# Kernel tuning notes

Hardware: AMD Instinct MI355X
Metric: run time of the kernel (lower is better)

## Reference

```python
import jax, jax.numpy as jnp
import numpy as np

INPUT_CHANNELS = 64
OUT_CHANNELS = 64
OUT_DIM = 4
IN_FEAT = INPUT_CHANNELS * OUT_DIM * 2   # 512
OUT_FEAT = OUT_CHANNELS * OUT_DIM        # 256
BATCH = 65536


def setup_inputs() -> dict:
    key = jax.random.key(0)
    k_x, k_w, k_b = jax.random.split(key, 3)
    x = jax.random.normal(k_x, (BATCH, IN_FEAT), dtype=jnp.float32)
    weight = jax.random.normal(k_w, (OUT_FEAT, IN_FEAT), dtype=jnp.float32)
    bias = jax.random.normal(k_b, (1, OUT_FEAT), dtype=jnp.float32)
    return {"x": x, "weight": weight, "bias": bias}


def reference(x, weight, bias) -> jnp.ndarray:
    # Original: (x[:, None] * weight).sum(-1) / sqrt(input_channels) + 0.1*bias
    # Mathematically identical to a GEMM: x @ weight.T
    scale = 1.0 / jnp.sqrt(jnp.asarray(INPUT_CHANNELS, dtype=x.dtype))
    out = jnp.einsum('bi,oi->bo', x, weight) * scale  # [B, out_feat]
    out = out + bias * 0.1
    return out
```

## Files before the change

kernel.cpp:

```cpp
#include <hip/hip_runtime.h>
#include <hip/hip_bf16.h>


typedef __bf16 bf16;
typedef __attribute__((ext_vector_type(8))) __bf16 bf16x8;
typedef __attribute__((ext_vector_type(4))) __bf16 bf16x4;
typedef __attribute__((ext_vector_type(4))) float f32x4;

#define BATCH_ 65536
#define KDIM   512
#define NDIM   256
#define NHALF  128
#define CHUNK_ROWS 16
#define CHUNKS 8
#define ROWS_PER_BLOCK (CHUNK_ROWS * CHUNKS)
#define OPAD 132

__global__ __launch_bounds__(256) void wcvt_kernel(const float* __restrict__ w,
                                                   bf16* __restrict__ wb) {
    int i = (blockIdx.x * 256 + threadIdx.x) * 4;
    f32x4 v = *(const f32x4*)(w + i);
    bf16x4 o;
    o[0] = (bf16)(v.x * 0.125f);
    o[1] = (bf16)(v.y * 0.125f);
    o[2] = (bf16)(v.z * 0.125f);
    o[3] = (bf16)(v.w * 0.125f);
    *(bf16x4*)(wb + i) = o;
}

__device__ __forceinline__ void stage_issue(const float* xc, int tid, f32x4 (&r)[4]) {
#pragma unroll
    for (int i = 0; i < 4; ++i)
        r[i] = *(const f32x4*)((const char*)xc + i * 8192 + tid * 16);
}

__device__ __forceinline__ void stage_write(bf16* buf, int tid, const f32x4 (&r)[4]) {
#pragma unroll
    for (int i = 0; i < 4; ++i) {
        const int row = i * 4 + (tid >> 7);
        const int off = (tid & 127) * 8;
        const int phys = row * 1024 + (off ^ ((row & 7) << 4));
        bf16x4 o;
        o[0] = (bf16)r[i].x;
        o[1] = (bf16)r[i].y;
        o[2] = (bf16)r[i].z;
        o[3] = (bf16)r[i].w;
        *(bf16x4*)((char*)buf + phys) = o;
    }
}

__device__ __forceinline__ void compute_chunk(const bf16* buf, const bf16x8 (&wf)[16],
                                              int l16, int q, f32x4& acc) {
    acc = (f32x4)0.0f;
    const char* base = (const char*)buf + l16 * 1024;
    const int xo = (l16 & 7) << 4;
#pragma unroll
    for (int kc = 0; kc < 16; ++kc) {
        bf16x8 a = *(const bf16x8*)(base + ((kc * 64 + q * 16) ^ xo));
        acc = __builtin_amdgcn_mfma_f32_16x16x32_bf16(a, wf[kc], acc, 0, 0, 0);
    }
}

__device__ __forceinline__ void owrite(float* ob, int w, int l16, int q,
                                       const f32x4& acc) {
    float* p = ob + (q * 4) * OPAD + w * 16 + l16;
#pragma unroll
    for (int rr = 0; rr < 4; ++rr)
        p[rr * OPAD] = acc[rr];
}

__device__ __forceinline__ void ostore(const float* ob, float* __restrict__ out,
                                       long row0, int half, int tid,
                                       const f32x4& bvv) {
    const int r2 = tid >> 5;
    const int c4 = (tid & 31) * 4;
    f32x4 v = *(const f32x4*)(ob + r2 * OPAD + c4);
    v.x += bvv.x; v.y += bvv.y; v.z += bvv.z; v.w += bvv.w;
    *(f32x4*)(out + (row0 + r2) * NDIM + half * NHALF + c4) = v;
}

__device__ __forceinline__ void lds_barrier() {
    asm volatile("s_waitcnt lgkmcnt(0)" ::: "memory");
    __builtin_amdgcn_s_barrier();
    __builtin_amdgcn_sched_barrier(0);
}

__global__ __launch_bounds__(512, 4) void gemm_kernel(const float* __restrict__ x,
                                                      const bf16* __restrict__ wb,
                                                      const float* __restrict__ bias,
                                                      float* __restrict__ out) {
    __shared__ __align__(16) bf16 bufA[CHUNK_ROWS * KDIM];
    __shared__ __align__(16) bf16 bufB[CHUNK_ROWS * KDIM];
    __shared__ __align__(16) float obuf0[CHUNK_ROWS * OPAD];
    __shared__ __align__(16) float obuf1[CHUNK_ROWS * OPAD];

    const int tid  = threadIdx.x;
    const int lane = tid & 63;
    const int w    = tid >> 6;
    const int q    = lane >> 4;
    const int l16  = lane & 15;

    const int g    = blockIdx.x;
    const int half = (g >> 3) & 1;
    const long rb  = (long)((g & 7) | ((g >> 4) << 3));
    const int n0   = half * NHALF + w * 16;
    const long row_base = rb * ROWS_PER_BLOCK;

    bf16x8 wf[16];
#pragma unroll
    for (int kc = 0; kc < 16; ++kc)
        wf[kc] = *(const bf16x8*)(wb + (long)(n0 + l16) * KDIM + kc * 32 + q * 8);

    f32x4 bvv;
    {
        f32x4 b = *(const f32x4*)(bias + half * NHALF + (tid & 31) * 4);
        bvv.x = 0.1f * b.x; bvv.y = 0.1f * b.y;
        bvv.z = 0.1f * b.z; bvv.w = 0.1f * b.w;
    }

    const float* xblk = x + row_base * KDIM;

    f32x4 r[4];
    stage_issue(xblk, tid, r);
    stage_write(bufA, tid, r);
    lds_barrier();

    f32x4 acc;
#pragma unroll 1
    for (int t = 0; t < CHUNKS; t += 2) {
        if (t + 1 < CHUNKS)
            stage_issue(xblk + (long)(t + 1) * CHUNK_ROWS * KDIM, tid, r);
        compute_chunk(bufA, wf, l16, q, acc);
        owrite(obuf0, w, l16, q, acc);
        if (t + 1 < CHUNKS)
            stage_write(bufB, tid, r);
        lds_barrier();
        ostore(obuf0, out, row_base + (long)t * CHUNK_ROWS, half, tid, bvv);

        if (t + 2 < CHUNKS)
            stage_issue(xblk + (long)(t + 2) * CHUNK_ROWS * KDIM, tid, r);
        compute_chunk(bufB, wf, l16, q, acc);
        owrite(obuf1, w, l16, q, acc);
        if (t + 2 < CHUNKS)
            stage_write(bufA, tid, r);
        lds_barrier();
        ostore(obuf1, out, row_base + (long)(t + 1) * CHUNK_ROWS, half, tid, bvv);
    }
}

extern "C" void kernel_launch(void* const* d_in, const int* in_sizes, int n_in,
                              void* d_out, int out_size, void* d_ws, size_t ws_size,
                              hipStream_t stream) {
    const float* x    = (const float*)d_in[0];
    const float* w    = (const float*)d_in[1];
    const float* bias = (const float*)d_in[2];
    float* out = (float*)d_out;
    bf16* wb   = (bf16*)d_ws;

    wcvt_kernel<<<(NDIM * KDIM) / (256 * 4), 256, 0, stream>>>(w, wb);
    gemm_kernel<<<(BATCH_ / ROWS_PER_BLOCK) * 2, 512, 0, stream>>>(x, wb, bias, out);
}
```

Before: 223.4 us.

## Halve block threads; each wave computes two 16-col N tiles

Blocks shrink from 512 to 256 threads, and each wave now covers 32 output columns with two MFMA accumulators. Each A fragment read from LDS is reused for two MFMAs, which halves LDS reads per MFMA. Staging switches to 32-byte loads per thread with bf16x8 LDS writes, and the output store loops over two rows. The cost is twice the weight registers per thread (wf[16][2]), and fewer waves per block may cut latency hiding, which launch_bounds(256,2) tries to offset.

New measurement: 225.0 us. No clear change (+0.7%).

```diff
diff --git a/kernel.cpp b/kernel.cpp
--- a/kernel.cpp
+++ b/kernel.cpp
@@ -28,55 +28,65 @@
     *(bf16x4*)(wb + i) = o;
 }
 
-__device__ __forceinline__ void stage_issue(const float* xc, int tid, f32x4 (&r)[4]) {
+__device__ __forceinline__ void stage_issue(const float* xc, int tid, f32x4 (&r)[8]) {
 #pragma unroll
-    for (int i = 0; i < 4; ++i)
-        r[i] = *(const f32x4*)((const char*)xc + i * 8192 + tid * 16);
-}
-
-__device__ __forceinline__ void stage_write(bf16* buf, int tid, const f32x4 (&r)[4]) {
-#pragma unroll
-    for (int i = 0; i < 4; ++i) {
-        const int row = i * 4 + (tid >> 7);
-        const int off = (tid & 127) * 8;
-        const int phys = row * 1024 + (off ^ ((row & 7) << 4));
-        bf16x4 o;
-        o[0] = (bf16)r[i].x;
-        o[1] = (bf16)r[i].y;
-        o[2] = (bf16)r[i].z;
-        o[3] = (bf16)r[i].w;
-        *(bf16x4*)((char*)buf + phys) = o;
+    for (int j = 0; j < 4; ++j) {
+        r[2 * j]     = *(const f32x4*)((const char*)xc + j * 8192 + tid * 32);
+        r[2 * j + 1] = *(const f32x4*)((const char*)xc + j * 8192 + tid * 32 + 16);
     }
 }
 
-__device__ __forceinline__ void compute_chunk(const bf16* buf, const bf16x8 (&wf)[16],
-                                              int l16, int q, f32x4& acc) {
-    acc = (f32x4)0.0f;
+__device__ __forceinline__ void stage_write(bf16* buf, int tid, const f32x4 (&r)[8]) {
+#pragma unroll
+    for (int j = 0; j < 4; ++j) {
+        const int row = j * 4 + (tid >> 6);
+        const int off = (tid & 63) * 16;
+        const int phys = row * 1024 + (off ^ ((row & 7) << 4));
+        bf16x8 o;
+        o[0] = (bf16)r[2 * j].x;     o[1] = (bf16)r[2 * j].y;
+        o[2] = (bf16)r[2 * j].z;     o[3] = (bf16)r[2 * j].w;
+        o[4] = (bf16)r[2 * j + 1].x; o[5] = (bf16)r[2 * j + 1].y;
+        o[6] = (bf16)r[2 * j + 1].z; o[7] = (bf16)r[2 * j + 1].w;
+        *(bf16x8*)((char*)buf + phys) = o;
+    }
+}
+
+__device__ __forceinline__ void compute_chunk(const bf16* buf, const bf16x8 (&wf)[16][2],
+                                              int l16, int q, f32x4 (&acc)[2]) {
+    acc[0] = (f32x4)0.0f;
+    acc[1] = (f32x4)0.0f;
     const char* base = (const char*)buf + l16 * 1024;
     const int xo = (l16 & 7) << 4;
 #pragma unroll
     for (int kc = 0; kc < 16; ++kc) {
         bf16x8 a = *(const bf16x8*)(base + ((kc * 64 + q * 16) ^ xo));
-        acc = __builtin_amdgcn_mfma_f32_16x16x32_bf16(a, wf[kc], acc, 0, 0, 0);
+        acc[0] = __builtin_amdgcn_mfma_f32_16x16x32_bf16(a, wf[kc][0], acc[0], 0, 0, 0);
+        acc[1] = __builtin_amdgcn_mfma_f32_16x16x32_bf16(a, wf[kc][1], acc[1], 0, 0, 0);
     }
 }
 
 __device__ __forceinline__ void owrite(float* ob, int w, int l16, int q,
-                                       const f32x4& acc) {
-    float* p = ob + (q * 4) * OPAD + w * 16 + l16;
+                                       const f32x4 (&acc)[2]) {
 #pragma unroll
-    for (int rr = 0; rr < 4; ++rr)
-        p[rr * OPAD] = acc[rr];
+    for (int nt = 0; nt < 2; ++nt) {
+        float* p = ob + (q * 4) * OPAD + w * 32 + nt * 16 + l16;
+#pragma unroll
+        for (int rr = 0; rr < 4; ++rr)
+            p[rr * OPAD] = acc[nt][rr];
+    }
 }
 
 __device__ __forceinline__ void ostore(const float* ob, float* __restrict__ out,
                                        long row0, int half, int tid,
                                        const f32x4& bvv) {
-    const int r2 = tid >> 5;
     const int c4 = (tid & 31) * 4;
-    f32x4 v = *(const f32x4*)(ob + r2 * OPAD + c4);
-    v.x += bvv.x; v.y += bvv.y; v.z += bvv.z; v.w += bvv.w;
-    *(f32x4*)(out + (row0 + r2) * NDIM + half * NHALF + c4) = v;
+#pragma unroll
+    for (int rr = 0; rr < 2; ++rr) {
+        const int r2 = (tid >> 5) + rr * 8;
+        f32x4 v = *(const f32x4*)(ob + r2 * OPAD + c4);
+        v.x += bvv.x; v.y += bvv.y; v.z += bvv.z; v.w += bvv.w;
+        *(f32x4*)(out + (row0 + r2) * NDIM + half * NHALF + c4) = v;
+    }
 }
 
 __device__ __forceinline__ void lds_barrier() {
@@ -85,7 +95,7 @@
     __builtin_amdgcn_sched_barrier(0);
 }
 
-__global__ __launch_bounds__(512, 4) void gemm_kernel(const float* __restrict__ x,
+__global__ __launch_bounds__(256, 2) void gemm_kernel(const float* __restrict__ x,
                                                       const bf16* __restrict__ wb,
                                                       const float* __restrict__ bias,
                                                       float* __restrict__ out) {
@@ -103,13 +113,16 @@
     const int g    = blockIdx.x;
     const int half = (g >> 3) & 1;
     const long rb  = (long)((g & 7) | ((g >> 4) << 3));
-    const int n0   = half * NHALF + w * 16;
+    const int n0   = half * NHALF + w * 32;
     const long row_base = rb * ROWS_PER_BLOCK;
 
-    bf16x8 wf[16];
+    bf16x8 wf[16][2];
 #pragma unroll
     for (int kc = 0; kc < 16; ++kc)
-        wf[kc] = *(const bf16x8*)(wb + (long)(n0 + l16) * KDIM + kc * 32 + q * 8);
+#pragma unroll
+        for (int nt = 0; nt < 2; ++nt)
+            wf[kc][nt] = *(const bf16x8*)(wb + (long)(n0 + nt * 16 + l16) * KDIM
+                                             + kc * 32 + q * 8);
 
     f32x4 bvv;
     {
@@ -120,12 +133,12 @@
 
     const float* xblk = x + row_base * KDIM;
 
-    f32x4 r[4];
+    f32x4 r[8];
     stage_issue(xblk, tid, r);
     stage_write(bufA, tid, r);
     lds_barrier();
 
-    f32x4 acc;
+    f32x4 acc[2];
 #pragma unroll 1
     for (int t = 0; t < CHUNKS; t += 2) {
         if (t + 1 < CHUNKS)
@@ -158,5 +171,5 @@
     bf16* wb   = (bf16*)d_ws;
 
     wcvt_kernel<<<(NDIM * KDIM) / (256 * 4), 256, 0, stream>>>(w, wb);
-    gemm_kernel<<<(BATCH_ / ROWS_PER_BLOCK) * 2, 512, 0, stream>>>(x, wb, bias, out);
+    gemm_kernel<<<(BATCH_ / ROWS_PER_BLOCK) * 2, 256, 0, stream>>>(x, wb, bias, out);
 }
```
